# Kernel tuning notes

Hardware: AMD Instinct MI355X
Metric: run time of the kernel (lower is better)

## Reference

```python
import jax, jax.numpy as jnp
import numpy as np

NUM_NODES = 50000
NUM_HYPEREDGES = 10000
NUM_INCIDENCES = 800000
CHANNELS = 256
NEG_SLOPE = 0.01  # torch leaky_relu default negative_slope


def setup_inputs() -> dict:
    key = jax.random.key(0)
    k_n, k_e, k_emb, k_cw, k_lw, k_lb = jax.random.split(key, 6)
    node_idx = jax.random.randint(k_n, (NUM_INCIDENCES,), 0, NUM_NODES, dtype=jnp.int32)
    edge_idx = jax.random.randint(k_e, (NUM_INCIDENCES,), 0, NUM_HYPEREDGES, dtype=jnp.int32)
    edge_index = jnp.stack([node_idx, edge_idx], axis=0)  # [2, nnz] incidence list
    s = 1.0 / np.sqrt(CHANNELS).astype(np.float32)
    emb = jax.random.normal(k_emb, (NUM_NODES, CHANNELS), jnp.float32)  # Node2Vec embedding table
    conv_w = jax.random.normal(k_cw, (CHANNELS, CHANNELS), jnp.float32) * s  # HypergraphConv.lin (no bias)
    conv_b = jnp.zeros((CHANNELS,), jnp.float32)  # HypergraphConv.bias
    lin_w = jax.random.normal(k_lw, (CHANNELS, CHANNELS), jnp.float32) * s
    lin_b = jax.random.normal(k_lb, (CHANNELS,), jnp.float32) * s
    return {"emb": emb, "conv_w": conv_w, "conv_b": conv_b,
            "lin_w": lin_w, "lin_b": lin_b, "edge_index": edge_index}


def reference(emb, conv_w, conv_b, lin_w, lin_b, edge_index):
    node_idx, edge_idx = edge_index[0], edge_index[1]
    # HypergraphConv (use_attention=False): X' = D^-1 H B^-1 H^T (X W^T) + b
    x = emb @ conv_w.T  # [N, C]
    ones = jnp.ones((NUM_INCIDENCES,), x.dtype)
    D = jax.ops.segment_sum(ones, node_idx, num_segments=NUM_NODES)       # node degree
    Dinv = jnp.where(D > 0, 1.0 / D, 0.0)
    B = jax.ops.segment_sum(ones, edge_idx, num_segments=NUM_HYPEREDGES)  # hyperedge degree
    Binv = jnp.where(B > 0, 1.0 / B, 0.0)
    # node -> hyperedge aggregation
    e = jax.ops.segment_sum(x[node_idx], edge_idx, num_segments=NUM_HYPEREDGES) * Binv[:, None]  # [E, C]
    # hyperedge -> node aggregation
    n = jax.ops.segment_sum(e[edge_idx], node_idx, num_segments=NUM_NODES) * Dinv[:, None] + conv_b  # [N, C]
    y = jax.nn.leaky_relu(n, NEG_SLOPE)
    g = y.T @ y  # [C, C] Gram
    out = jax.nn.leaky_relu(g @ lin_w.T + lin_b, NEG_SLOPE)
    return out
```

## Files before the change

### kernel.cpp

```cpp
#include <hip/hip_runtime.h>

#define N_NODES 50000
#define N_EDGES 10000
#define NNZ     800000
#define C       256
#define SLOPE   0.01f
#define KTOT    50176
#define KCHUNK  512
#define NZB     98
#define MPAD    10048

#define NB      250
#define EB_E    40
#define EB_N    200
#define CHUNK   3125
#define CAP     6000

#define OFF_CC_E    0
#define OFF_CC_N    1024
#define OFF_CUR_E   2048
#define OFF_CUR_N   3072
#define ZERO_BYTES  4096
#define OFF_CB_E    266240
#define OFF_CB_N    267264
#define OFF_RS_N    268288
#define OFF_RS_E    468480
#define OFF_BUF_E   508672
#define OFF_BUF_N   3708672
#define OFF_CSR_E   6908672
#define OFF_CSR_N   10108672
#define OFF_EMBH    13308672
#define OFF_YT      13308672
#define OFF_EACC    39000064
#define OFF_E2      44144640
#define OFF_CWH     49289216
#define OFF_PART    49420288

typedef __attribute__((ext_vector_type(8))) short short8;
typedef __attribute__((ext_vector_type(4))) float floatx4;

static __device__ __forceinline__ unsigned short f2bf(float f) {
    unsigned int u = __float_as_uint(f);
    u = (u + 0x7fffu + ((u >> 16) & 1u)) >> 16;
    return (unsigned short)u;
}

static __device__ __forceinline__ void acc_bf8(const uint4 d, float* a) {
    a[0] += __uint_as_float(d.x << 16);
    a[1] += __uint_as_float(d.x & 0xffff0000u);
    a[2] += __uint_as_float(d.y << 16);
    a[3] += __uint_as_float(d.y & 0xffff0000u);
    a[4] += __uint_as_float(d.z << 16);
    a[5] += __uint_as_float(d.z & 0xffff0000u);
    a[6] += __uint_as_float(d.w << 16);
    a[7] += __uint_as_float(d.w & 0xffff0000u);
}

static __device__ __forceinline__ void gather4(const uint4* __restrict__ tbl4,
                                               const int* __restrict__ csr,
                                               int s, int t, int half, int l32,
                                               int zrow, float* a) {
    for (int i = s + half; i < t; i += 8) {
        int e0 = csr[i];
        int e1 = (i + 2 < t) ? csr[i + 2] : zrow;
        int e2 = (i + 4 < t) ? csr[i + 4] : zrow;
        int e3 = (i + 6 < t) ? csr[i + 6] : zrow;
        uint4 d0 = tbl4[(size_t)e0 * 32 + l32];
        uint4 d1 = tbl4[(size_t)e1 * 32 + l32];
        uint4 d2 = tbl4[(size_t)e2 * 32 + l32];
        uint4 d3 = tbl4[(size_t)e3 * 32 + l32];
        acc_bf8(d0, a); acc_bf8(d1, a); acc_bf8(d2, a); acc_bf8(d3, a);
    }
}

static __device__ __forceinline__ void gather8(const uint4* __restrict__ tbl4,
                                               const int* __restrict__ csr,
                                               int s, int t, int half, int l32,
                                               int zrow, float* a) {
    for (int i = s + half; i < t; i += 16) {
        int e0 = csr[i];
        int e1 = (i + 2  < t) ? csr[i + 2]  : zrow;
        int e2 = (i + 4  < t) ? csr[i + 4]  : zrow;
        int e3 = (i + 6  < t) ? csr[i + 6]  : zrow;
        int e4 = (i + 8  < t) ? csr[i + 8]  : zrow;
        int e5 = (i + 10 < t) ? csr[i + 10] : zrow;
        int e6 = (i + 12 < t) ? csr[i + 12] : zrow;
        int e7 = (i + 14 < t) ? csr[i + 14] : zrow;
        uint4 d0 = tbl4[(size_t)e0 * 32 + l32];
        uint4 d1 = tbl4[(size_t)e1 * 32 + l32];
        uint4 d2 = tbl4[(size_t)e2 * 32 + l32];
        uint4 d3 = tbl4[(size_t)e3 * 32 + l32];
        uint4 d4 = tbl4[(size_t)e4 * 32 + l32];
        uint4 d5 = tbl4[(size_t)e5 * 32 + l32];
        uint4 d6 = tbl4[(size_t)e6 * 32 + l32];
        uint4 d7 = tbl4[(size_t)e7 * 32 + l32];
        acc_bf8(d0, a); acc_bf8(d1, a); acc_bf8(d2, a); acc_bf8(d3, a);
        acc_bf8(d4, a); acc_bf8(d5, a); acc_bf8(d6, a); acc_bf8(d7, a);
    }
}

__global__ __launch_bounds__(256) void zero_kernel(float4* __restrict__ p, int n4) {
    int i = blockIdx.x * 256 + threadIdx.x;
    if (i < n4) p[i] = make_float4(0.f, 0.f, 0.f, 0.f);
}

#define PREP_EMB_BLOCKS 6251
#define PREP_CW_BLOCKS  32
__global__ __launch_bounds__(256) void prep_kernel(const float4* __restrict__ emb4,
                                                   uint4* __restrict__ embh4,
                                                   const float4* __restrict__ cw4,
                                                   uint4* __restrict__ cwh4,
                                                   const int* __restrict__ node_idx,
                                                   const int* __restrict__ edge_idx,
                                                   int* __restrict__ cc_e,
                                                   int* __restrict__ cc_n) {
    __shared__ int he[NB], hn[NB];
    int b = blockIdx.x, tid = threadIdx.x;
    if (b < PREP_EMB_BLOCKS) {
        int i = b * 256 + tid;
        if (i >= 1600032) return;
        uint4 o = {0u, 0u, 0u, 0u};
        if (i < 1600000) {
            float4 f0 = emb4[2 * i], f1 = emb4[2 * i + 1];
            o.x = f2bf(f0.x) | ((unsigned)f2bf(f0.y) << 16);
            o.y = f2bf(f0.z) | ((unsigned)f2bf(f0.w) << 16);
            o.z = f2bf(f1.x) | ((unsigned)f2bf(f1.y) << 16);
            o.w = f2bf(f1.z) | ((unsigned)f2bf(f1.w) << 16);
        }
        embh4[i] = o;
    } else if (b < PREP_EMB_BLOCKS + PREP_CW_BLOCKS) {
        int i = (b - PREP_EMB_BLOCKS) * 256 + tid;
        float4 f0 = cw4[2 * i], f1 = cw4[2 * i + 1];
        uint4 o;
        o.x = f2bf(f0.x) | ((unsigned)f2bf(f0.y) << 16);
        o.y = f2bf(f0.z) | ((unsigned)f2bf(f0.w) << 16);
        o.z = f2bf(f1.x) | ((unsigned)f2bf(f1.y) << 16);
        o.w = f2bf(f1.z) | ((unsigned)f2bf(f1.w) << 16);
        cwh4[i] = o;
    } else {
        int base = (b - PREP_EMB_BLOCKS - PREP_CW_BLOCKS) * CHUNK;
        for (int i = tid; i < NB; i += 256) { he[i] = 0; hn[i] = 0; }
        __syncthreads();
        for (int i = tid; i < CHUNK; i += 256) {
            atomicAdd(&he[edge_idx[base + i] / EB_E], 1);
            atomicAdd(&hn[node_idx[base + i] / EB_N], 1);
        }
        __syncthreads();
        for (int k = tid; k < NB; k += 256) {
            if (he[k]) atomicAdd(&cc_e[k], he[k]);
            if (hn[k]) atomicAdd(&cc_n[k], hn[k]);
        }
    }
}

__global__ __launch_bounds__(256) void coarse_scan_kernel(const int* __restrict__ cc_e,
                                                          const int* __restrict__ cc_n,
                                                          int* __restrict__ cb_e,
                                                          int* __restrict__ cb_n) {
    __shared__ int tmp[256];
    int tid = threadIdx.x;
    int v = (tid < NB) ? cc_e[tid] : 0;
    tmp[tid] = v;
    __syncthreads();
    for (int off = 1; off < 256; off <<= 1) {
        int t = (tid >= off) ? tmp[tid - off] : 0;
        __syncthreads();
        tmp[tid] += t;
        __syncthreads();
    }
    if (tid < NB) cb_e[tid + 1] = tmp[tid];
    if (tid == 0) cb_e[0] = 0;
    __syncthreads();
    v = (tid < NB) ? cc_n[tid] : 0;
    tmp[tid] = v;
    __syncthreads();
    for (int off = 1; off < 256; off <<= 1) {
        int t = (tid >= off) ? tmp[tid - off] : 0;
        __syncthreads();
        tmp[tid] += t;
        __syncthreads();
    }
    if (tid < NB) cb_n[tid + 1] = tmp[tid];
    if (tid == 0) cb_n[0] = 0;
}

__global__ __launch_bounds__(256) void bucket_scatter_kernel(const int* __restrict__ node_idx,
                                                             const int* __restrict__ edge_idx,
                                                             const int* __restrict__ cb_e,
                                                             const int* __restrict__ cb_n,
                                                             int* __restrict__ cur_e,
                                                             int* __restrict__ cur_n,
                                                             int* __restrict__ buf_e,
                                                             int* __restrict__ buf_n) {
    __shared__ int he[NB], hn[NB], be[NB], bn[NB];
    int tid = threadIdx.x;
    int base = blockIdx.x * CHUNK;
    for (int i = tid; i < NB; i += 256) { he[i] = 0; hn[i] = 0; }
    __syncthreads();
    int pe[13], pn[13];
    #pragma unroll
    for (int k = 0; k < 13; k++) {
        int i = tid + k * 256;
        if (i < CHUNK) {
            int e = edge_idx[base + i], v = node_idx[base + i];
            int ke = e / EB_E, kn = v / EB_N;
            pe[k] = (ke << 12) | atomicAdd(&he[ke], 1);
            pn[k] = (kn << 12) | atomicAdd(&hn[kn], 1);
        }
    }
    __syncthreads();
    for (int k = tid; k < NB; k += 256) {
        int c = he[k];
        be[k] = cb_e[k] + (c ? atomicAdd(&cur_e[k], c) : 0);
        int cn = hn[k];
        bn[k] = cb_n[k] + (cn ? atomicAdd(&cur_n[k], cn) : 0);
    }
    __syncthreads();
    #pragma unroll
    for (int k = 0; k < 13; k++) {
        int i = tid + k * 256;
        if (i < CHUNK) {
            int e = edge_idx[base + i], v = node_idx[base + i];
            int ke = pe[k] >> 12, oe = pe[k] & 4095;
            buf_e[be[ke] + oe] = (v << 6) | (e - ke * EB_E);
            int kn = pn[k] >> 12, on = pn[k] & 4095;
            buf_n[bn[kn] + on] = (e << 8) | (v - kn * EB_N);
        }
    }
}

__global__ __launch_bounds__(256) void bucket_sort_kernel(const int* __restrict__ buf_e,
                                                          const int* __restrict__ buf_n,
                                                          const int* __restrict__ cb_e,
                                                          const int* __restrict__ cb_n,
                                                          int* __restrict__ csr_e,
                                                          int* __restrict__ csr_n,
                                                          int* __restrict__ rs_e,
                                                          int* __restrict__ rs_n) {
    __shared__ int A[CAP];
    __shared__ int h[EB_N], bs[EB_N];
    int tid = threadIdx.x;
    bool edgeSide = blockIdx.x < NB;
    int k = edgeSide ? blockIdx.x : blockIdx.x - NB;
    int eb = edgeSide ? EB_E : EB_N;
    int shift = edgeSide ? 6 : 8;
    int mask = (1 << shift) - 1;
    const int* cb  = edgeSide ? cb_e : cb_n;
    const int* buf = edgeSide ? buf_e : buf_n;
    int* csr       = edgeSide ? csr_e : csr_n;
    int* rs        = edgeSide ? rs_e : rs_n;
    int base = cb[k];
    int cnt = cb[k + 1] - base;
    for (int i = tid; i < eb; i += 256) h[i] = 0;
    __syncthreads();
    for (int i = tid; i < cnt; i += 256) {
        int it = buf[base + i];
        if (i < CAP) A[i] = it;
        atomicAdd(&h[it & mask], 1);
    }
    __syncthreads();
    if (tid == 0) {
        int s = 0;
        for (int j = 0; j < eb; j++) { bs[j] = s; s += h[j]; }
    }
    __syncthreads();
    for (int j = tid; j < eb; j += 256) {
        rs[k * eb + j] = base + bs[j];
        h[j] = 0;
    }
    if (tid == 0 && k == NB - 1) rs[edgeSide ? N_EDGES : N_NODES] = NNZ;
    __syncthreads();
    for (int i = tid; i < cnt; i += 256) {
        int it = (i < CAP) ? A[i] : buf[base + i];
        int loc = it & mask;
        int off = bs[loc] + atomicAdd(&h[loc], 1);
        csr[base + off] = it >> shift;
    }
}

__global__ __launch_bounds__(256) void edge_aggregate_kernel(const uint4* __restrict__ embh4,
                                                             const int* __restrict__ csr_e,
                                                             const int* __restrict__ rs_e,
                                                             unsigned short* __restrict__ e_acc_h) {
    int e = blockIdx.x * 4 + (threadIdx.x >> 6);
    int lane = threadIdx.x & 63;
    int half = lane >> 5, l32 = lane & 31;
    int s = 0, t = 0;
    if (e < N_EDGES) { s = rs_e[e]; t = rs_e[e + 1]; }
    float a[8] = {0.f, 0.f, 0.f, 0.f, 0.f, 0.f, 0.f, 0.f};
    gather8(embh4, csr_e, s, t, half, l32, N_NODES, a);
    #pragma unroll
    for (int j = 0; j < 8; j++) a[j] += __shfl_xor(a[j], 32);
    if (half == 0) {
        uint4 o;
        o.x = f2bf(a[0]) | ((unsigned)f2bf(a[1]) << 16);
        o.y = f2bf(a[2]) | ((unsigned)f2bf(a[3]) << 16);
        o.z = f2bf(a[4]) | ((unsigned)f2bf(a[5]) << 16);
        o.w = f2bf(a[6]) | ((unsigned)f2bf(a[7]) << 16);
        ((uint4*)(e_acc_h + (size_t)e * C))[l32] = o;
    }
}

__global__ __launch_bounds__(256) void edge_gemm_mfma_kernel(const unsigned short* __restrict__ e_acc_h,
                                                             const unsigned short* __restrict__ cwh,
                                                             const int* __restrict__ rs_e,
                                                             unsigned short* __restrict__ e2h) {
    __shared__ __align__(16) unsigned short As[64 * 72];
    __shared__ __align__(16) unsigned short Bs[64 * 72];
    int i0 = blockIdx.x * 64, j0 = blockIdx.y * 64;
    int tid = threadIdx.x;
    int w = tid >> 6, lane = tid & 63;
    int col = lane & 15, quad = lane >> 4;
    floatx4 acc[4] = {};
    for (int step = 0; step < 4; step++) {
        int kb = step * 64;
        __syncthreads();
        #pragma unroll
        for (int l = 0; l < 2; l++) {
            int slot = tid + l * 256;
            int row = slot >> 3, grp = slot & 7;
            uint4 da = *(const uint4*)(e_acc_h + (size_t)(i0 + row) * C + kb + grp * 8);
            *(uint4*)(&As[row * 72 + grp * 8]) = da;
            uint4 db = *(const uint4*)(cwh + (size_t)(j0 + row) * C + kb + grp * 8);
            *(uint4*)(&Bs[row * 72 + grp * 8]) = db;
        }
        __syncthreads();
        #pragma unroll
        for (int sub = 0; sub < 2; sub++) {
            short8 a = *(const short8*)(&As[(w * 16 + col) * 72 + sub * 32 + quad * 8]);
            #pragma unroll
            for (int jt = 0; jt < 4; jt++) {
                short8 b = *(const short8*)(&Bs[(jt * 16 + col) * 72 + sub * 32 + quad * 8]);
                acc[jt] = __builtin_amdgcn_mfma_f32_16x16x32_bf16(a, b, acc[jt], 0, 0, 0);
            }
        }
    }
    #pragma unroll
    for (int r = 0; r < 4; r++) {
        int m = i0 + w * 16 + quad * 4 + r;
        int deg = (m < N_EDGES) ? rs_e[m + 1] - rs_e[m] : 0;
        float binv = (deg > 0) ? 1.0f / (float)deg : 0.0f;
        #pragma unroll
        for (int jt = 0; jt < 4; jt++)
            e2h[(size_t)m * C + j0 + jt * 16 + col] = f2bf(acc[jt][r] * binv);
    }
}

__global__ __launch_bounds__(256) void node_aggregate_t_kernel(const uint4* __restrict__ e2h4,
                                                               const int* __restrict__ csr_n,
                                                               const int* __restrict__ rs_n,
                                                               const float* __restrict__ conv_b,
                                                               unsigned short* __restrict__ yT) {
    __shared__ __align__(16) unsigned short T[32][256];
    int n0 = blockIdx.x * 32;
    int tid = threadIdx.x;
    int w = tid >> 6, lane = tid & 63;
    int half = lane >> 5, l32 = lane & 31;
    int base = n0 + w * 8;
    int rsv = rs_n[min(base + lane, N_NODES)];
    float4 b0 = ((const float4*)conv_b)[l32 * 2];
    float4 b1 = ((const float4*)conv_b)[l32 * 2 + 1];
    float bb[8] = {b0.x, b0.y, b0.z, b0.w, b1.x, b1.y, b1.z, b1.w};
    for (int q = 0; q < 8; q++) {
        int v = base + q;
        int s = __shfl(rsv, q), t = __shfl(rsv, q + 1);
        float a[8] = {0.f, 0.f, 0.f, 0.f, 0.f, 0.f, 0.f, 0.f};
        gather4(e2h4, csr_n, s, t, half, l32, N_EDGES, a);
        #pragma unroll
        for (int j = 0; j < 8; j++) a[j] += __shfl_xor(a[j], 32);
        float dinv = (t > s) ? 1.0f / (float)(t - s) : 0.0f;
        unsigned int pk[4];
        #pragma unroll
        for (int j = 0; j < 4; j++) {
            float r0 = a[2 * j] * dinv + bb[2 * j];
            float r1 = a[2 * j + 1] * dinv + bb[2 * j + 1];
            r0 = (r0 > 0.f) ? r0 : SLOPE * r0;
            r1 = (r1 > 0.f) ? r1 : SLOPE * r1;
            if (v >= N_NODES) { r0 = 0.f; r1 = 0.f; }
            pk[j] = f2bf(r0) | ((unsigned)f2bf(r1) << 16);
        }
        if (half == 0) {
            uint4 o; o.x = pk[0]; o.y = pk[1]; o.z = pk[2]; o.w = pk[3];
            *(uint4*)(&T[w * 8 + q][l32 * 8]) = o;
        }
    }
    __syncthreads();
    int ch = tid;
    #pragma unroll
    for (int jj = 0; jj < 4; jj++) {
        uint4 o;
        o.x = T[jj * 8 + 0][ch] | ((unsigned)T[jj * 8 + 1][ch] << 16);
        o.y = T[jj * 8 + 2][ch] | ((unsigned)T[jj * 8 + 3][ch] << 16);
        o.z = T[jj * 8 + 4][ch] | ((unsigned)T[jj * 8 + 5][ch] << 16);
        o.w = T[jj * 8 + 6][ch] | ((unsigned)T[jj * 8 + 7][ch] << 16);
        *(uint4*)(yT + (size_t)ch * KTOT + n0 + jj * 8) = o;
    }
}

__global__ __launch_bounds__(256) void gram_mfma_kernel(const unsigned short* __restrict__ yT,
                                                        float* __restrict__ part) {
    static const int PI[10] = {0, 0, 0, 0, 1, 1, 1, 2, 2, 3};
    static const int PJ[10] = {0, 1, 2, 3, 1, 2, 3, 2, 3, 3};
    __shared__ __align__(16) unsigned short As[64 * 72];
    __shared__ __align__(16) unsigned short Bs[64 * 72];
    int i0 = PI[blockIdx.x] * 64, j0 = PJ[blockIdx.x] * 64;
    bool diag = (i0 == j0);
    int kb0 = blockIdx.y * KCHUNK;
    int tid = threadIdx.x;
    int w = tid >> 6, lane = tid & 63;
    int col = lane & 15, quad = lane >> 4;
    floatx4 acc[4] = {};
    for (int step = 0; step < KCHUNK / 64; step++) {
        int kb = kb0 + step * 64;
        __syncthreads();
        #pragma unroll
        for (int l = 0; l < 2; l++) {
            int slot = tid + l * 256;
            int row = slot >> 3, grp = slot & 7;
            uint4 da = *(const uint4*)(yT + (size_t)(i0 + row) * KTOT + kb + grp * 8);
            *(uint4*)(&As[row * 72 + grp * 8]) = da;
            if (!diag) {
                uint4 db = *(const uint4*)(yT + (size_t)(j0 + row) * KTOT + kb + grp * 8);
                *(uint4*)(&Bs[row * 72 + grp * 8]) = db;
            }
        }
        __syncthreads();
        const unsigned short* Bb = diag ? As : Bs;
        #pragma unroll
        for (int sub = 0; sub < 2; sub++) {
            short8 a = *(const short8*)(&As[(w * 16 + col) * 72 + sub * 32 + quad * 8]);
            #pragma unroll
            for (int jt = 0; jt < 4; jt++) {
                short8 b = *(const short8*)(&Bb[(jt * 16 + col) * 72 + sub * 32 + quad * 8]);
                acc[jt] = __builtin_amdgcn_mfma_f32_16x16x32_bf16(a, b, acc[jt], 0, 0, 0);
            }
        }
    }
    float* slab = part + ((size_t)blockIdx.y * 10 + blockIdx.x) * 4096;
    #pragma unroll
    for (int jt = 0; jt < 4; jt++)
        #pragma unroll
        for (int r = 0; r < 4; r++)
            slab[(w * 16 + quad * 4 + r) * 64 + jt * 16 + col] = acc[jt][r];
}

__global__ __launch_bounds__(256) void greduce_out_kernel(const float* __restrict__ part,
                                                          const float* __restrict__ lin_w,
                                                          const float* __restrict__ lin_b,
                                                          float* __restrict__ out) {
    __shared__ float gs[C];
    int i = blockIdx.x, j = threadIdx.x;
    int a = i >> 6, b = j >> 6;
    int lo = min(a, b), hi = max(a, b);
    int t = lo * (7 - lo) / 2 + hi;
    int li = (a <= b) ? (i & 63) : (j & 63);
    int lj = (a <= b) ? (j & 63) : (i & 63);
    const float* p = part + (size_t)t * 4096 + li * 64 + lj;
    float s = 0.f;
    for (int z = 0; z < NZB; z++) s += p[(size_t)z * 40960];
    gs[j] = s;
    __syncthreads();
    float acc = lin_b[j];
    const float* wrow = lin_w + (size_t)j * C;
    for (int k = 0; k < C; k++) acc += gs[k] * wrow[k];
    out[(size_t)i * C + j] = (acc > 0.f) ? acc : SLOPE * acc;
}

extern "C" void kernel_launch(void* const* d_in, const int* in_sizes, int n_in,
                              void* d_out, int out_size, void* d_ws, size_t ws_size,
                              hipStream_t stream) {
    const float* emb    = (const float*)d_in[0];
    const float* conv_w = (const float*)d_in[1];
    const float* conv_b = (const float*)d_in[2];
    const float* lin_w  = (const float*)d_in[3];
    const float* lin_b  = (const float*)d_in[4];
    const int*   eidx   = (const int*)d_in[5];
    const int* node_idx = eidx;
    const int* edge_idx = eidx + NNZ;

    char* ws = (char*)d_ws;
    int* cc_e  = (int*)(ws + OFF_CC_E);
    int* cc_n  = (int*)(ws + OFF_CC_N);
    int* cur_e = (int*)(ws + OFF_CUR_E);
    int* cur_n = (int*)(ws + OFF_CUR_N);
    int* cb_e  = (int*)(ws + OFF_CB_E);
    int* cb_n  = (int*)(ws + OFF_CB_N);
    int* rs_n  = (int*)(ws + OFF_RS_N);
    int* rs_e  = (int*)(ws + OFF_RS_E);
    int* buf_e = (int*)(ws + OFF_BUF_E);
    int* buf_n = (int*)(ws + OFF_BUF_N);
    int* csr_e = (int*)(ws + OFF_CSR_E);
    int* csr_n = (int*)(ws + OFF_CSR_N);
    uint4* embh4 = (uint4*)(ws + OFF_EMBH);
    unsigned short* e_acc_h = (unsigned short*)(ws + OFF_EACC);
    unsigned short* e2h = (unsigned short*)(ws + OFF_E2);
    unsigned short* cwh = (unsigned short*)(ws + OFF_CWH);
    unsigned short* yT  = (unsigned short*)(ws + OFF_YT);
    float* part = (float*)(ws + OFF_PART);
    float* out = (float*)d_out;

    zero_kernel<<<1, 256, 0, stream>>>((float4*)ws, ZERO_BYTES / 16);

    prep_kernel<<<PREP_EMB_BLOCKS + PREP_CW_BLOCKS + 256, 256, 0, stream>>>(
        (const float4*)emb, embh4, (const float4*)conv_w, (uint4*)cwh,
        node_idx, edge_idx, cc_e, cc_n);

    coarse_scan_kernel<<<1, 256, 0, stream>>>(cc_e, cc_n, cb_e, cb_n);

    bucket_scatter_kernel<<<256, 256, 0, stream>>>(node_idx, edge_idx, cb_e, cb_n,
                                                   cur_e, cur_n, buf_e, buf_n);

    bucket_sort_kernel<<<2 * NB, 256, 0, stream>>>(buf_e, buf_n, cb_e, cb_n,
                                                   csr_e, csr_n, rs_e, rs_n);

    edge_aggregate_kernel<<<MPAD / 4, 256, 0, stream>>>(embh4, csr_e, rs_e, e_acc_h);

    edge_gemm_mfma_kernel<<<dim3(MPAD / 64, C / 64), 256, 0, stream>>>(e_acc_h, cwh, rs_e, e2h);

    node_aggregate_t_kernel<<<KTOT / 32, 256, 0, stream>>>((const uint4*)e2h, csr_n, rs_n,
                                                           conv_b, yT);

    gram_mfma_kernel<<<dim3(10, NZB), 256, 0, stream>>>(yT, part);

    greduce_out_kernel<<<C, 256, 0, stream>>>(part, lin_w, lin_b, out);
}
```

Baseline: 300.5 us.

## Channel-slice gather tables and 16-bit CSR indices for both aggregation passes

The bf16 embedding table and the edge-message table are re-laid out as 8 channel slices of 32 channels each. Each aggregation block handles one slice, so every gathered row segment is 64 bytes and the tables a block touches are smaller, which should improve L2 hit rates for the random gathers. CSR neighbour indices are stored as unsigned short, halving index traffic; this relies on node and edge ids fitting in 16 bits after the bucket offset encoding. The node aggregation now uses one quad of lanes per node with a smaller LDS transpose. The cost is more blocks and more total index reads, since each slice re-reads the CSR.

After: 282.4 us. 6.0% less time.

```diff
diff --git a/kernel.cpp b/kernel.cpp
--- a/kernel.cpp
+++ b/kernel.cpp
@@ -15,6 +15,9 @@
 #define EB_N    200
 #define CHUNK   3125
 #define CAP     6000
+
+#define EAGG_G  252
+#define NAGG_G  784
 
 #define OFF_CC_E    0
 #define OFF_CC_N    1024
@@ -54,49 +57,6 @@
     a[5] += __uint_as_float(d.z & 0xffff0000u);
     a[6] += __uint_as_float(d.w << 16);
     a[7] += __uint_as_float(d.w & 0xffff0000u);
-}
-
-static __device__ __forceinline__ void gather4(const uint4* __restrict__ tbl4,
-                                               const int* __restrict__ csr,
-                                               int s, int t, int half, int l32,
-                                               int zrow, float* a) {
-    for (int i = s + half; i < t; i += 8) {
-        int e0 = csr[i];
-        int e1 = (i + 2 < t) ? csr[i + 2] : zrow;
-        int e2 = (i + 4 < t) ? csr[i + 4] : zrow;
-        int e3 = (i + 6 < t) ? csr[i + 6] : zrow;
-        uint4 d0 = tbl4[(size_t)e0 * 32 + l32];
-        uint4 d1 = tbl4[(size_t)e1 * 32 + l32];
-        uint4 d2 = tbl4[(size_t)e2 * 32 + l32];
-        uint4 d3 = tbl4[(size_t)e3 * 32 + l32];
-        acc_bf8(d0, a); acc_bf8(d1, a); acc_bf8(d2, a); acc_bf8(d3, a);
-    }
-}
-
-static __device__ __forceinline__ void gather8(const uint4* __restrict__ tbl4,
-                                               const int* __restrict__ csr,
-                                               int s, int t, int half, int l32,
-                                               int zrow, float* a) {
-    for (int i = s + half; i < t; i += 16) {
-        int e0 = csr[i];
-        int e1 = (i + 2  < t) ? csr[i + 2]  : zrow;
-        int e2 = (i + 4  < t) ? csr[i + 4]  : zrow;
-        int e3 = (i + 6  < t) ? csr[i + 6]  : zrow;
-        int e4 = (i + 8  < t) ? csr[i + 8]  : zrow;
-        int e5 = (i + 10 < t) ? csr[i + 10] : zrow;
-        int e6 = (i + 12 < t) ? csr[i + 12] : zrow;
-        int e7 = (i + 14 < t) ? csr[i + 14] : zrow;
-        uint4 d0 = tbl4[(size_t)e0 * 32 + l32];
-        uint4 d1 = tbl4[(size_t)e1 * 32 + l32];
-        uint4 d2 = tbl4[(size_t)e2 * 32 + l32];
-        uint4 d3 = tbl4[(size_t)e3 * 32 + l32];
-        uint4 d4 = tbl4[(size_t)e4 * 32 + l32];
-        uint4 d5 = tbl4[(size_t)e5 * 32 + l32];
-        uint4 d6 = tbl4[(size_t)e6 * 32 + l32];
-        uint4 d7 = tbl4[(size_t)e7 * 32 + l32];
-        acc_bf8(d0, a); acc_bf8(d1, a); acc_bf8(d2, a); acc_bf8(d3, a);
-        acc_bf8(d4, a); acc_bf8(d5, a); acc_bf8(d6, a); acc_bf8(d7, a);
-    }
 }
 
 __global__ __launch_bounds__(256) void zero_kernel(float4* __restrict__ p, int n4) {
@@ -127,7 +87,8 @@
             o.z = f2bf(f1.x) | ((unsigned)f2bf(f1.y) << 16);
             o.w = f2bf(f1.z) | ((unsigned)f2bf(f1.w) << 16);
         }
-        embh4[i] = o;
+        int node = i >> 5, c = i & 31;
+        embh4[(size_t)(((c >> 2) * 50001 + node) << 2) + (c & 3)] = o;
     } else if (b < PREP_EMB_BLOCKS + PREP_CW_BLOCKS) {
         int i = (b - PREP_EMB_BLOCKS) * 256 + tid;
         float4 f0 = cw4[2 * i], f1 = cw4[2 * i + 1];
@@ -233,8 +194,8 @@
                                                           const int* __restrict__ buf_n,
                                                           const int* __restrict__ cb_e,
                                                           const int* __restrict__ cb_n,
-                                                          int* __restrict__ csr_e,
-                                                          int* __restrict__ csr_n,
+                                                          unsigned short* __restrict__ csr_e,
+                                                          unsigned short* __restrict__ csr_n,
                                                           int* __restrict__ rs_e,
                                                           int* __restrict__ rs_n) {
     __shared__ int A[CAP];
@@ -247,7 +208,7 @@
     int mask = (1 << shift) - 1;
     const int* cb  = edgeSide ? cb_e : cb_n;
     const int* buf = edgeSide ? buf_e : buf_n;
-    int* csr       = edgeSide ? csr_e : csr_n;
+    unsigned short* csr = edgeSide ? csr_e : csr_n;
     int* rs        = edgeSide ? rs_e : rs_n;
     int base = cb[k];
     int cnt = cb[k + 1] - base;
@@ -274,30 +235,46 @@
         int it = (i < CAP) ? A[i] : buf[base + i];
         int loc = it & mask;
         int off = bs[loc] + atomicAdd(&h[loc], 1);
-        csr[base + off] = it >> shift;
+        csr[base + off] = (unsigned short)(it >> shift);
     }
 }
 
 __global__ __launch_bounds__(256) void edge_aggregate_kernel(const uint4* __restrict__ embh4,
-                                                             const int* __restrict__ csr_e,
+                                                             const unsigned short* __restrict__ csr_e,
                                                              const int* __restrict__ rs_e,
                                                              unsigned short* __restrict__ e_acc_h) {
-    int e = blockIdx.x * 4 + (threadIdx.x >> 6);
-    int lane = threadIdx.x & 63;
-    int half = lane >> 5, l32 = lane & 31;
-    int s = 0, t = 0;
-    if (e < N_EDGES) { s = rs_e[e]; t = rs_e[e + 1]; }
-    float a[8] = {0.f, 0.f, 0.f, 0.f, 0.f, 0.f, 0.f, 0.f};
-    gather8(embh4, csr_e, s, t, half, l32, N_NODES, a);
-    #pragma unroll
-    for (int j = 0; j < 8; j++) a[j] += __shfl_xor(a[j], 32);
-    if (half == 0) {
-        uint4 o;
-        o.x = f2bf(a[0]) | ((unsigned)f2bf(a[1]) << 16);
-        o.y = f2bf(a[2]) | ((unsigned)f2bf(a[3]) << 16);
-        o.z = f2bf(a[4]) | ((unsigned)f2bf(a[5]) << 16);
-        o.w = f2bf(a[6]) | ((unsigned)f2bf(a[7]) << 16);
-        ((uint4*)(e_acc_h + (size_t)e * C))[l32] = o;
+    int sid = blockIdx.x & 7, g = blockIdx.x >> 3;
+    const uint4* __restrict__ tbl = embh4 + (size_t)sid * 50001 * 4;
+    int tid = threadIdx.x;
+    int w = tid >> 6, lane = tid & 63;
+    int q = lane >> 2, c4 = lane & 3;
+    int ebase = g * 40 + w * 10;
+    for (int j = 0; j < 10; j++) {
+        int e = ebase + j;
+        if (e >= MPAD) return;
+        int s = 0, t = 0;
+        if (e < N_EDGES) { s = rs_e[e]; t = rs_e[e + 1]; }
+        float a[8] = {0.f, 0.f, 0.f, 0.f, 0.f, 0.f, 0.f, 0.f};
+        for (int i = s + q; i < t; i += 32) {
+            int n0 = csr_e[i];
+            int n1 = (i + 16 < t) ? (int)csr_e[i + 16] : N_NODES;
+            uint4 d0 = tbl[n0 * 4 + c4];
+            uint4 d1 = tbl[n1 * 4 + c4];
+            acc_bf8(d0, a); acc_bf8(d1, a);
+        }
+        #pragma unroll
+        for (int off = 4; off < 64; off <<= 1) {
+            #pragma unroll
+            for (int jj = 0; jj < 8; jj++) a[jj] += __shfl_xor(a[jj], off);
+        }
+        if (q == 0) {
+            uint4 o;
+            o.x = f2bf(a[0]) | ((unsigned)f2bf(a[1]) << 16);
+            o.y = f2bf(a[2]) | ((unsigned)f2bf(a[3]) << 16);
+            o.z = f2bf(a[4]) | ((unsigned)f2bf(a[5]) << 16);
+            o.w = f2bf(a[6]) | ((unsigned)f2bf(a[7]) << 16);
+            ((uint4*)(e_acc_h + (size_t)e * C + sid * 32))[c4] = o;
+        }
     }
 }
 
@@ -341,60 +318,54 @@
         int deg = (m < N_EDGES) ? rs_e[m + 1] - rs_e[m] : 0;
         float binv = (deg > 0) ? 1.0f / (float)deg : 0.0f;
         #pragma unroll
-        for (int jt = 0; jt < 4; jt++)
-            e2h[(size_t)m * C + j0 + jt * 16 + col] = f2bf(acc[jt][r] * binv);
+        for (int jt = 0; jt < 4; jt++) {
+            int ch = j0 + jt * 16 + col;
+            e2h[(size_t)((ch >> 5) * MPAD + m) * 32 + (ch & 31)] = f2bf(acc[jt][r] * binv);
+        }
     }
 }
 
 __global__ __launch_bounds__(256) void node_aggregate_t_kernel(const uint4* __restrict__ e2h4,
-                                                               const int* __restrict__ csr_n,
+                                                               const unsigned short* __restrict__ csr_n,
                                                                const int* __restrict__ rs_n,
                                                                const float* __restrict__ conv_b,
                                                                unsigned short* __restrict__ yT) {
-    __shared__ __align__(16) unsigned short T[32][256];
-    int n0 = blockIdx.x * 32;
+    __shared__ unsigned short T[32][66];
+    int sid = blockIdx.x & 7, g = blockIdx.x >> 3;
+    const uint4* __restrict__ tbl = e2h4 + (size_t)sid * MPAD * 4;
     int tid = threadIdx.x;
     int w = tid >> 6, lane = tid & 63;
-    int half = lane >> 5, l32 = lane & 31;
-    int base = n0 + w * 8;
-    int rsv = rs_n[min(base + lane, N_NODES)];
-    float4 b0 = ((const float4*)conv_b)[l32 * 2];
-    float4 b1 = ((const float4*)conv_b)[l32 * 2 + 1];
+    int q = lane >> 2, c4 = lane & 3;
+    int n = g * 64 + w * 16 + q;
+    int s = 0, t = 0;
+    if (n < N_NODES) { s = rs_n[n]; t = rs_n[n + 1]; }
+    float4 b0 = ((const float4*)conv_b)[sid * 8 + c4 * 2];
+    float4 b1 = ((const float4*)conv_b)[sid * 8 + c4 * 2 + 1];
+    float a[8] = {0.f, 0.f, 0.f, 0.f, 0.f, 0.f, 0.f, 0.f};
+    for (int i = s; i < t; i += 2) {
+        int r0 = csr_n[i];
+        int r1 = (i + 1 < t) ? (int)csr_n[i + 1] : N_EDGES;
+        uint4 d0 = tbl[r0 * 4 + c4];
+        uint4 d1 = tbl[r1 * 4 + c4];
+        acc_bf8(d0, a); acc_bf8(d1, a);
+    }
+    float dinv = (t > s) ? 1.0f / (float)(t - s) : 0.0f;
     float bb[8] = {b0.x, b0.y, b0.z, b0.w, b1.x, b1.y, b1.z, b1.w};
-    for (int q = 0; q < 8; q++) {
-        int v = base + q;
-        int s = __shfl(rsv, q), t = __shfl(rsv, q + 1);
-        float a[8] = {0.f, 0.f, 0.f, 0.f, 0.f, 0.f, 0.f, 0.f};
-        gather4(e2h4, csr_n, s, t, half, l32, N_EDGES, a);
-        #pragma unroll
-        for (int j = 0; j < 8; j++) a[j] += __shfl_xor(a[j], 32);
-        float dinv = (t > s) ? 1.0f / (float)(t - s) : 0.0f;
-        unsigned int pk[4];
-        #pragma unroll
-        for (int j = 0; j < 4; j++) {
-            float r0 = a[2 * j] * dinv + bb[2 * j];
-            float r1 = a[2 * j + 1] * dinv + bb[2 * j + 1];
-            r0 = (r0 > 0.f) ? r0 : SLOPE * r0;
-            r1 = (r1 > 0.f) ? r1 : SLOPE * r1;
-            if (v >= N_NODES) { r0 = 0.f; r1 = 0.f; }
-            pk[j] = f2bf(r0) | ((unsigned)f2bf(r1) << 16);
-        }
-        if (half == 0) {
-            uint4 o; o.x = pk[0]; o.y = pk[1]; o.z = pk[2]; o.w = pk[3];
-            *(uint4*)(&T[w * 8 + q][l32 * 8]) = o;
-        }
-    }
-    __syncthreads();
-    int ch = tid;
     #pragma unroll
-    for (int jj = 0; jj < 4; jj++) {
-        uint4 o;
-        o.x = T[jj * 8 + 0][ch] | ((unsigned)T[jj * 8 + 1][ch] << 16);
-        o.y = T[jj * 8 + 2][ch] | ((unsigned)T[jj * 8 + 3][ch] << 16);
-        o.z = T[jj * 8 + 4][ch] | ((unsigned)T[jj * 8 + 5][ch] << 16);
-        o.w = T[jj * 8 + 6][ch] | ((unsigned)T[jj * 8 + 7][ch] << 16);
-        *(uint4*)(yT + (size_t)ch * KTOT + n0 + jj * 8) = o;
-    }
+    for (int jj = 0; jj < 8; jj++) {
+        float r = a[jj] * dinv + bb[jj];
+        r = (r > 0.f) ? r : SLOPE * r;
+        if (n >= N_NODES) r = 0.f;
+        T[c4 * 8 + jj][w * 16 + q] = f2bf(r);
+    }
+    __syncthreads();
+    int rr = tid >> 3, cc = tid & 7;
+    uint4 o;
+    o.x = T[rr][cc * 8 + 0] | ((unsigned)T[rr][cc * 8 + 1] << 16);
+    o.y = T[rr][cc * 8 + 2] | ((unsigned)T[rr][cc * 8 + 3] << 16);
+    o.z = T[rr][cc * 8 + 4] | ((unsigned)T[rr][cc * 8 + 5] << 16);
+    o.w = T[rr][cc * 8 + 6] | ((unsigned)T[rr][cc * 8 + 7] << 16);
+    *(uint4*)(yT + (size_t)(sid * 32 + rr) * KTOT + g * 64 + cc * 8) = o;
 }
 
 __global__ __launch_bounds__(256) void gram_mfma_kernel(const unsigned short* __restrict__ yT,
@@ -489,8 +460,8 @@
     int* rs_e  = (int*)(ws + OFF_RS_E);
     int* buf_e = (int*)(ws + OFF_BUF_E);
     int* buf_n = (int*)(ws + OFF_BUF_N);
-    int* csr_e = (int*)(ws + OFF_CSR_E);
-    int* csr_n = (int*)(ws + OFF_CSR_N);
+    unsigned short* csr_e = (unsigned short*)(ws + OFF_CSR_E);
+    unsigned short* csr_n = (unsigned short*)(ws + OFF_CSR_N);
     uint4* embh4 = (uint4*)(ws + OFF_EMBH);
     unsigned short* e_acc_h = (unsigned short*)(ws + OFF_EACC);
     unsigned short* e2h = (unsigned short*)(ws + OFF_E2);
@@ -513,12 +484,12 @@
     bucket_sort_kernel<<<2 * NB, 256, 0, stream>>>(buf_e, buf_n, cb_e, cb_n,
                                                    csr_e, csr_n, rs_e, rs_n);
 
-    edge_aggregate_kernel<<<MPAD / 4, 256, 0, stream>>>(embh4, csr_e, rs_e, e_acc_h);
+    edge_aggregate_kernel<<<8 * EAGG_G, 256, 0, stream>>>(embh4, csr_e, rs_e, e_acc_h);
 
     edge_gemm_mfma_kernel<<<dim3(MPAD / 64, C / 64), 256, 0, stream>>>(e_acc_h, cwh, rs_e, e2h);
 
-    node_aggregate_t_kernel<<<KTOT / 32, 256, 0, stream>>>((const uint4*)e2h, csr_n, rs_n,
-                                                           conv_b, yT);
+    node_aggregate_t_kernel<<<8 * NAGG_G, 256, 0, stream>>>((const uint4*)e2h, csr_n, rs_n,
+                                                            conv_b, yT);
 
     gram_mfma_kernel<<<dim3(10, NZB), 256, 0, stream>>>(yT, part);
 
```
